# Performance work log

Hardware: AMD Instinct MI355X
Metric: run time of the kernel (lower is better)

## Reference

```python
import jax, jax.numpy as jnp
import numpy as np

HIDDEN = 4096
NUM_HEADS = 32
HEAD_DIM = HIDDEN // NUM_HEADS


def _fp8_roundtrip(x):
    # emulate torch float8_e4m3fn weight storage
    return x.astype(jnp.float8_e4m3fn).astype(jnp.float32)


def setup_inputs() -> dict:
    key = jax.random.key(0)
    ks = jax.random.split(key, 10)
    B, S = 2, 4096
    hidden_states = jax.random.normal(ks[0], (B, S, HIDDEN), dtype=jnp.float32)
    scale = 0.02
    def lin(kw, kb):
        w = jax.random.normal(kw, (HIDDEN, HIDDEN), dtype=jnp.float32) * scale
        b = jax.random.normal(kb, (HIDDEN,), dtype=jnp.float32) * scale
        return w, b
    wq, bq = lin(ks[1], ks[2])
    wk, bk = lin(ks[3], ks[4])
    wv, bv = lin(ks[5], ks[6])
    wl, bl = lin(ks[7], ks[8])
    # fp8-quantized Q/K/V projections (latent projection stays fp32)
    wq, bq = _fp8_roundtrip(wq), _fp8_roundtrip(bq)
    wk, bk = _fp8_roundtrip(wk), _fp8_roundtrip(bk)
    wv, bv = _fp8_roundtrip(wv), _fp8_roundtrip(bv)
    return {"hidden_states": hidden_states, "wq": wq, "bq": bq, "wk": wk,
            "bk": bk, "wv": wv, "bv": bv, "wl": wl, "bl": bl}


def reference(hidden_states, wq, bq, wk, bk, wv, bv, wl, bl):
    B, S, E = hidden_states.shape
    H, D = NUM_HEADS, HEAD_DIM
    q = (hidden_states @ wq.T + bq).reshape(B, S, H, D)
    k = (hidden_states @ wk.T + bk).reshape(B, S, H, D)
    v = (hidden_states @ wv.T + bv).reshape(B, S, H, D)
    latent = hidden_states @ wl.T + bl  # computed but unused, as in source
    # NOTE: source does NOT transpose to [B,H,S,D]; scores are [B,S,H,H]
    scores = jnp.einsum('bshd,bstd->bsht', q, k) / np.sqrt(D).astype(np.float32)
    probs = jax.nn.softmax(scores, axis=-1)
    context = jnp.einsum('bsht,bstd->bshd', probs, v).reshape(B, S, E)
    return context
```

## Files before the change

kernel.cpp:

```cpp
#include <hip/hip_runtime.h>
#include <stdint.h>

#define HIDDEN 4096
#define M_TOK 8192
#define KDIM 4096

typedef __attribute__((ext_vector_type(8))) __bf16 bf16x8;
typedef __attribute__((ext_vector_type(4))) float f32x4;
typedef __attribute__((ext_vector_type(8))) unsigned short u16x8;

#define GAS __attribute__((address_space(1)))
#define LAS __attribute__((address_space(3)))

__device__ __forceinline__ unsigned short f2bf(float f) {
  unsigned int u = __float_as_uint(f);
  u += 0x7FFFu + ((u >> 16) & 1u);
  return (unsigned short)(u >> 16);
}
__device__ __forceinline__ float bf2f(unsigned short b) {
  return __uint_as_float(((unsigned int)b) << 16);
}

__global__ __launch_bounds__(256) void cvt_kernel(const float* __restrict__ in,
                                                  unsigned short* __restrict__ out,
                                                  int n8) {
  int i = blockIdx.x * 256 + threadIdx.x;
  if (i >= n8) return;
  const f32x4* p = (const f32x4*)in + (size_t)2 * i;
  f32x4 a = p[0], b = p[1];
  u16x8 o;
  o[0] = f2bf(a.x); o[1] = f2bf(a.y); o[2] = f2bf(a.z); o[3] = f2bf(a.w);
  o[4] = f2bf(b.x); o[5] = f2bf(b.y); o[6] = f2bf(b.z); o[7] = f2bf(b.w);
  ((u16x8*)out)[i] = o;
}

#define BAR() __builtin_amdgcn_s_barrier()
#define PRIO(p) __builtin_amdgcn_s_setprio(p)
#define VMC6() asm volatile("s_waitcnt vmcnt(6)" ::: "memory")
#define VMC4() asm volatile("s_waitcnt vmcnt(4)" ::: "memory")
#define VMC0() asm volatile("s_waitcnt vmcnt(0)" ::: "memory")
#define PH_MID() do { __builtin_amdgcn_s_barrier(); \
  asm volatile("s_waitcnt lgkmcnt(0)" ::: "memory"); \
  __builtin_amdgcn_sched_barrier(0); } while (0)

__global__ __launch_bounds__(512, 2) void gemm_qkv(
    const unsigned short* __restrict__ A,
    const unsigned short* __restrict__ W,
    const float* __restrict__ bias,
    unsigned short* __restrict__ out) {
  __shared__ __attribute__((aligned(16))) unsigned short lds[65536];

  int tid = threadIdx.x;
  int lane = tid & 63;
  int w = tid >> 6;
  int wm = w >> 2;
  int wn = w & 3;
  int l16 = lane & 15;
  int lk = lane >> 4;

  int bid = blockIdx.x;
  int wg = (bid & 7) * 192 + (bid >> 3);
  int tm = wg / 48;
  int tn = wg - tm * 48;
  int m0 = tm << 8, n0 = tn << 8;

  int rp = tid >> 3;
  int ce = ((tid & 7) << 3) ^ ((rp & 7) << 3);
  const unsigned short* aSrc = A + (size_t)(m0 + rp) * KDIM + ce;
  const unsigned short* bSrc = W + (size_t)(n0 + rp) * KDIM + ce;
  int tid8 = tid * 8;

#define STA(b, h, kt) do { \
  __builtin_amdgcn_global_load_lds((GAS void*)(aSrc + (size_t)((h)*128) * KDIM + (kt)*64), \
      (LAS void*)(lds + (b)*16384 + (h)*8192 + tid8), 16, 0, 0); \
  __builtin_amdgcn_global_load_lds((GAS void*)(aSrc + (size_t)((h)*128 + 64) * KDIM + (kt)*64), \
      (LAS void*)(lds + (b)*16384 + (h)*8192 + 4096 + tid8), 16, 0, 0); } while (0)
#define STB(b, h, kt) do { \
  __builtin_amdgcn_global_load_lds((GAS void*)(bSrc + (size_t)((h)*128) * KDIM + (kt)*64), \
      (LAS void*)(lds + 32768 + (b)*16384 + (h)*8192 + tid8), 16, 0, 0); \
  __builtin_amdgcn_global_load_lds((GAS void*)(bSrc + (size_t)((h)*128 + 64) * KDIM + (kt)*64), \
      (LAS void*)(lds + 32768 + (b)*16384 + (h)*8192 + 4096 + tid8), 16, 0, 0); } while (0)

  int colbase = (lk << 3) ^ ((l16 & 7) << 3);
  int aRd = wm * 8192 + l16 * 64 + colbase;
  int bRd = (wn >> 1) * 8192 + (wn & 1) * 4096 + l16 * 64 + colbase;

#define RD_A(c, mi, ks) (*(const bf16x8*)(lds + (c)*16384 + (((aRd) + (mi)*1024) ^ ((ks)*32))))
#define RD_B(c, nj, ks) (*(const bf16x8*)(lds + 32768 + (c)*16384 + (((bRd) + (nj)*1024) ^ ((ks)*32))))

  bf16x8 av[8][2];
  bf16x8 bv[4][2];
  f32x4 acc[8][4] = {};

#define RP1(c) do { \
  bv[0][0]=RD_B(c,0,0); bv[0][1]=RD_B(c,0,1); bv[1][0]=RD_B(c,1,0); bv[1][1]=RD_B(c,1,1); \
  bv[2][0]=RD_B(c,2,0); bv[2][1]=RD_B(c,2,1); bv[3][0]=RD_B(c,3,0); bv[3][1]=RD_B(c,3,1); \
  av[0][0]=RD_A(c,0,0); av[0][1]=RD_A(c,0,1); av[1][0]=RD_A(c,1,0); av[1][1]=RD_A(c,1,1); } while (0)
#define RP2(c) do { \
  av[2][0]=RD_A(c,2,0); av[2][1]=RD_A(c,2,1); av[3][0]=RD_A(c,3,0); av[3][1]=RD_A(c,3,1); \
  av[4][0]=RD_A(c,4,0); av[4][1]=RD_A(c,4,1); av[5][0]=RD_A(c,5,0); av[5][1]=RD_A(c,5,1); } while (0)
#define RP3(c) do { \
  av[6][0]=RD_A(c,6,0); av[6][1]=RD_A(c,6,1); av[7][0]=RD_A(c,7,0); av[7][1]=RD_A(c,7,1); } while (0)

#define MFMA2(mi, nj) do { \
  acc[mi][nj] = __builtin_amdgcn_mfma_f32_16x16x32_bf16(av[mi][0], bv[nj][0], acc[mi][nj], 0, 0, 0); \
  acc[mi][nj] = __builtin_amdgcn_mfma_f32_16x16x32_bf16(av[mi][1], bv[nj][1], acc[mi][nj], 0, 0, 0); } while (0)
#define MM(mi) do { MFMA2(mi,0); MFMA2(mi,1); MFMA2(mi,2); MFMA2(mi,3); } while (0)

  STB(0, 0, 0); STB(0, 1, 0); STA(0, 0, 0); STA(0, 1, 0);
  VMC4();
  STB(1, 0, 1); STB(1, 1, 1); STA(1, 0, 1);
  VMC6();
  BAR();

  for (int it = 0; it < 31; ++it) {
    int k1 = 2 * it + 1, k2 = 2 * it + 2, k3 = 2 * it + 3;
    RP1(0); STA(1, 1, k1); PH_MID(); PRIO(1); MM(0); MM(1); PRIO(0); BAR();
    RP2(0); STB(0, 0, k2); PH_MID(); PRIO(1); MM(2); MM(3); PRIO(0); BAR();
    RP3(0); STB(0, 1, k2); PH_MID(); PRIO(1); MM(4); MM(5); PRIO(0); BAR();
            STA(0, 0, k2); PH_MID(); PRIO(1); MM(6); MM(7); PRIO(0); VMC6(); BAR();
    RP1(1); STA(0, 1, k2); PH_MID(); PRIO(1); MM(0); MM(1); PRIO(0); BAR();
    RP2(1); STB(1, 0, k3); PH_MID(); PRIO(1); MM(2); MM(3); PRIO(0); BAR();
    RP3(1); STB(1, 1, k3); PH_MID(); PRIO(1); MM(4); MM(5); PRIO(0); BAR();
            STA(1, 0, k3); PH_MID(); PRIO(1); MM(6); MM(7); PRIO(0); VMC6(); BAR();
  }
  RP1(0); STA(1, 1, 63); PH_MID(); PRIO(1); MM(0); MM(1); PRIO(0); BAR();
  RP2(0);                PH_MID(); PRIO(1); MM(2); MM(3); PRIO(0); BAR();
  RP3(0);                PH_MID(); PRIO(1); MM(4); MM(5); PRIO(0); BAR();
                         PH_MID(); PRIO(1); MM(6); MM(7); PRIO(0); VMC0(); BAR();
  RP1(1);                PH_MID(); PRIO(1); MM(0); MM(1); PRIO(0); BAR();
  RP2(1);                PH_MID(); PRIO(1); MM(2); MM(3); PRIO(0); BAR();
  RP3(1);                PH_MID(); PRIO(1); MM(4); MM(5); PRIO(0); BAR();
                         PH_MID(); PRIO(1); MM(6); MM(7); PRIO(0);

  int matc = n0 >> 12;
  int ncol = (n0 & 4095) + wn * 64;
  unsigned short* O = out + (size_t)matc * M_TOK * HIDDEN;
  float bb[4];
#pragma unroll
  for (int nj = 0; nj < 4; ++nj) bb[nj] = bias[n0 + wn * 64 + nj * 16 + l16];
#pragma unroll
  for (int mi = 0; mi < 8; ++mi) {
#pragma unroll
    for (int r = 0; r < 4; ++r) {
      int row = m0 + wm * 128 + mi * 16 + lk * 4 + r;
      size_t rb = (size_t)row * HIDDEN + ncol + l16;
#pragma unroll
      for (int nj = 0; nj < 4; ++nj)
        O[rb + nj * 16] = f2bf(acc[mi][nj][r] + bb[nj]);
    }
  }
}

__global__ __launch_bounds__(256) void attn_kernel(const unsigned short* __restrict__ qkv,
                                                   float* __restrict__ out) {
  __shared__ float sQ[32 * 132];
  __shared__ float sK[32 * 132];
  __shared__ float sV[32 * 132];
  __shared__ float sP[32 * 33];

  int m = blockIdx.x;
  int tid = threadIdx.x;
  const unsigned short* gq = qkv + (size_t)m * HIDDEN;
  const unsigned short* gk = gq + (size_t)M_TOK * HIDDEN;
  const unsigned short* gv = gk + (size_t)M_TOK * HIDDEN;

  int row = tid >> 3;
  int cb = (tid & 7) << 4;
  int go = row * 128 + cb;
  int lo = row * 132 + cb;
  {
    u16x8 x0 = *(const u16x8*)(gq + go);
    u16x8 x1 = *(const u16x8*)(gq + go + 8);
#pragma unroll
    for (int j = 0; j < 8; ++j) { sQ[lo + j] = bf2f(x0[j]); sQ[lo + 8 + j] = bf2f(x1[j]); }
    x0 = *(const u16x8*)(gk + go);
    x1 = *(const u16x8*)(gk + go + 8);
#pragma unroll
    for (int j = 0; j < 8; ++j) { sK[lo + j] = bf2f(x0[j]); sK[lo + 8 + j] = bf2f(x1[j]); }
    x0 = *(const u16x8*)(gv + go);
    x1 = *(const u16x8*)(gv + go + 8);
#pragma unroll
    for (int j = 0; j < 8; ++j) { sV[lo + j] = bf2f(x0[j]); sV[lo + 8 + j] = bf2f(x1[j]); }
  }
  __syncthreads();

  int h = tid >> 3;
  int t4 = (tid & 7) << 2;
  const f32x4* qr = (const f32x4*)(sQ + h * 132);
  const f32x4* k0 = (const f32x4*)(sK + (t4 + 0) * 132);
  const f32x4* k1 = (const f32x4*)(sK + (t4 + 1) * 132);
  const f32x4* k2 = (const f32x4*)(sK + (t4 + 2) * 132);
  const f32x4* k3 = (const f32x4*)(sK + (t4 + 3) * 132);
  float s0 = 0.f, s1 = 0.f, s2 = 0.f, s3 = 0.f;
#pragma unroll
  for (int d = 0; d < 32; ++d) {
    f32x4 q = qr[d];
    f32x4 a = k0[d]; s0 += q.x * a.x + q.y * a.y + q.z * a.z + q.w * a.w;
    f32x4 b = k1[d]; s1 += q.x * b.x + q.y * b.y + q.z * b.z + q.w * b.w;
    f32x4 c = k2[d]; s2 += q.x * c.x + q.y * c.y + q.z * c.z + q.w * c.w;
    f32x4 e = k3[d]; s3 += q.x * e.x + q.y * e.y + q.z * e.z + q.w * e.w;
  }
  const float scale = 0.08838834764831845f;
  s0 *= scale; s1 *= scale; s2 *= scale; s3 *= scale;
  float mx = fmaxf(fmaxf(s0, s1), fmaxf(s2, s3));
  mx = fmaxf(mx, __shfl_xor(mx, 1));
  mx = fmaxf(mx, __shfl_xor(mx, 2));
  mx = fmaxf(mx, __shfl_xor(mx, 4));
  float e0 = __expf(s0 - mx), e1 = __expf(s1 - mx), e2 = __expf(s2 - mx), e3 = __expf(s3 - mx);
  float sum = e0 + e1 + e2 + e3;
  sum += __shfl_xor(sum, 1);
  sum += __shfl_xor(sum, 2);
  sum += __shfl_xor(sum, 4);
  float inv = 1.0f / sum;
  sP[h * 33 + t4 + 0] = e0 * inv;
  sP[h * 33 + t4 + 1] = e1 * inv;
  sP[h * 33 + t4 + 2] = e2 * inv;
  sP[h * 33 + t4 + 3] = e3 * inv;
  __syncthreads();

  int d0 = (tid & 7) << 4;
  f32x4 o0 = {0.f, 0.f, 0.f, 0.f}, o1 = o0, o2 = o0, o3 = o0;
  const float* pr = sP + h * 33;
#pragma unroll
  for (int t = 0; t < 32; ++t) {
    float p = pr[t];
    const f32x4* vr = (const f32x4*)(sV + t * 132 + d0);
    o0 += p * vr[0];
    o1 += p * vr[1];
    o2 += p * vr[2];
    o3 += p * vr[3];
  }
  f32x4* op = (f32x4*)(out + (size_t)m * HIDDEN + h * 128 + d0);
  op[0] = o0; op[1] = o1; op[2] = o2; op[3] = o3;
}

extern "C" void kernel_launch(void* const* d_in, const int* in_sizes, int n_in,
                              void* d_out, int out_size, void* d_ws, size_t ws_size,
                              hipStream_t stream) {
  const float* hs = (const float*)d_in[0];
  const float* wq = (const float*)d_in[1];
  const float* bq = (const float*)d_in[2];
  const float* wk = (const float*)d_in[3];
  const float* bk = (const float*)d_in[4];
  const float* wv = (const float*)d_in[5];
  const float* bv = (const float*)d_in[6];

  char* ws = (char*)d_ws;
  const size_t HS_OFF = 0;
  const size_t W_OFF = 67108864;
  const size_t QKV_OFF = 167772160;
  const size_t BIAS_OFF = 369098752;
  const size_t NEED = 369147904;
  if (ws_size < NEED) return;

  unsigned short* hsb = (unsigned short*)(ws + HS_OFF);
  unsigned short* wb = (unsigned short*)(ws + W_OFF);
  unsigned short* qkv = (unsigned short*)(ws + QKV_OFF);
  float* bias = (float*)(ws + BIAS_OFF);

  cvt_kernel<<<16384, 256, 0, stream>>>(hs, hsb, 4194304);
  cvt_kernel<<<8192, 256, 0, stream>>>(wq, wb, 2097152);
  cvt_kernel<<<8192, 256, 0, stream>>>(wk, wb + 16777216, 2097152);
  cvt_kernel<<<8192, 256, 0, stream>>>(wv, wb + 33554432, 2097152);
  hipMemcpyAsync(bias, bq, 16384, hipMemcpyDeviceToDevice, stream);
  hipMemcpyAsync(bias + 4096, bk, 16384, hipMemcpyDeviceToDevice, stream);
  hipMemcpyAsync(bias + 8192, bv, 16384, hipMemcpyDeviceToDevice, stream);

  gemm_qkv<<<1536, 512, 0, stream>>>(hsb, wb, bias, qkv);
  attn_kernel<<<8192, 256, 0, stream>>>(qkv, (float*)d_out);
}
```

Measured before the change: 896.6 us.

## Switch QKV GEMM from 16x16x32 to 32x32x16 bf16 MFMA tiles

```diff
diff --git a/kernel.cpp b/kernel.cpp
--- a/kernel.cpp
+++ b/kernel.cpp
@@ -7,6 +7,7 @@
 
 typedef __attribute__((ext_vector_type(8))) __bf16 bf16x8;
 typedef __attribute__((ext_vector_type(4))) float f32x4;
+typedef __attribute__((ext_vector_type(16))) float f32x16;
 typedef __attribute__((ext_vector_type(8))) unsigned short u16x8;
 
 #define GAS __attribute__((address_space(1)))
@@ -55,8 +56,9 @@
   int w = tid >> 6;
   int wm = w >> 2;
   int wn = w & 3;
-  int l16 = lane & 15;
-  int lk = lane >> 4;
+  int l31 = lane & 31;
+  int lg = lane >> 5;
+  int l7 = lane & 7;
 
   int bid = blockIdx.x;
   int wg = (bid & 7) * 192 + (bid >> 3);
@@ -81,31 +83,29 @@
   __builtin_amdgcn_global_load_lds((GAS void*)(bSrc + (size_t)((h)*128 + 64) * KDIM + (kt)*64), \
       (LAS void*)(lds + 32768 + (b)*16384 + (h)*8192 + 4096 + tid8), 16, 0, 0); } while (0)
 
-  int colbase = (lk << 3) ^ ((l16 & 7) << 3);
-  int aRd = wm * 8192 + l16 * 64 + colbase;
-  int bRd = (wn >> 1) * 8192 + (wn & 1) * 4096 + l16 * 64 + colbase;
-
-#define RD_A(c, mi, ks) (*(const bf16x8*)(lds + (c)*16384 + (((aRd) + (mi)*1024) ^ ((ks)*32))))
-#define RD_B(c, nj, ks) (*(const bf16x8*)(lds + 32768 + (c)*16384 + (((bRd) + (nj)*1024) ^ ((ks)*32))))
-
-  bf16x8 av[8][2];
-  bf16x8 bv[4][2];
-  f32x4 acc[8][4] = {};
-
-#define RP1(c) do { \
-  bv[0][0]=RD_B(c,0,0); bv[0][1]=RD_B(c,0,1); bv[1][0]=RD_B(c,1,0); bv[1][1]=RD_B(c,1,1); \
-  bv[2][0]=RD_B(c,2,0); bv[2][1]=RD_B(c,2,1); bv[3][0]=RD_B(c,3,0); bv[3][1]=RD_B(c,3,1); \
-  av[0][0]=RD_A(c,0,0); av[0][1]=RD_A(c,0,1); av[1][0]=RD_A(c,1,0); av[1][1]=RD_A(c,1,1); } while (0)
-#define RP2(c) do { \
-  av[2][0]=RD_A(c,2,0); av[2][1]=RD_A(c,2,1); av[3][0]=RD_A(c,3,0); av[3][1]=RD_A(c,3,1); \
-  av[4][0]=RD_A(c,4,0); av[4][1]=RD_A(c,4,1); av[5][0]=RD_A(c,5,0); av[5][1]=RD_A(c,5,1); } while (0)
-#define RP3(c) do { \
-  av[6][0]=RD_A(c,6,0); av[6][1]=RD_A(c,6,1); av[7][0]=RD_A(c,7,0); av[7][1]=RD_A(c,7,1); } while (0)
-
-#define MFMA2(mi, nj) do { \
-  acc[mi][nj] = __builtin_amdgcn_mfma_f32_16x16x32_bf16(av[mi][0], bv[nj][0], acc[mi][nj], 0, 0, 0); \
-  acc[mi][nj] = __builtin_amdgcn_mfma_f32_16x16x32_bf16(av[mi][1], bv[nj][1], acc[mi][nj], 0, 0, 0); } while (0)
-#define MM(mi) do { MFMA2(mi,0); MFMA2(mi,1); MFMA2(mi,2); MFMA2(mi,3); } while (0)
+  int aRd0 = wm * 8192 + l31 * 64 + ((lg ^ l7) << 3);
+  int aK0 = aRd0, aK1 = aRd0 ^ 16, aK2 = aRd0 ^ 32, aK3 = aRd0 ^ 48;
+  int bRd0 = (wn >> 1) * 8192 + (wn & 1) * 4096 + l31 * 64 + ((lg ^ l7) << 3);
+  int bK0 = bRd0, bK1 = bRd0 ^ 16, bK2 = bRd0 ^ 32, bK3 = bRd0 ^ 48;
+
+#define RA(c, mi, ks) avv[ks][mi] = *(const bf16x8*)(lds + (c)*16384 + aK##ks + (mi)*2048)
+#define RB(c, nj, ks) bvv[nj][ks] = *(const bf16x8*)(lds + 32768 + (c)*16384 + bK##ks + (nj)*2048)
+
+  bf16x8 avv[4][4];
+  bf16x8 bvv[2][4];
+  f32x16 acc[4][2] = {};
+
+#define MF(mi, nj, ks) acc[mi][nj] = __builtin_amdgcn_mfma_f32_32x32x16_bf16( \
+    avv[ks][mi], bvv[nj][ks], acc[mi][nj], 0, 0, 0)
+#define MMKS(ks) do { MF(0,0,ks); MF(0,1,ks); MF(1,0,ks); MF(1,1,ks); \
+                      MF(2,0,ks); MF(2,1,ks); MF(3,0,ks); MF(3,1,ks); } while (0)
+
+#define RP1(c) do { RB(c,0,0); RB(c,0,1); RB(c,0,2); RB(c,0,3); \
+                    RB(c,1,0); RB(c,1,1); RB(c,1,2); RB(c,1,3); \
+                    RA(c,0,0); RA(c,1,0); RA(c,2,0); RA(c,3,0); } while (0)
+#define RP2(c) do { RA(c,0,1); RA(c,1,1); RA(c,2,1); RA(c,3,1); \
+                    RA(c,0,2); RA(c,1,2); RA(c,2,2); RA(c,3,2); } while (0)
+#define RP3(c) do { RA(c,0,3); RA(c,1,3); RA(c,2,3); RA(c,3,3); } while (0)
 
   STB(0, 0, 0); STB(0, 1, 0); STA(0, 0, 0); STA(0, 1, 0);
   VMC4();
@@ -115,39 +115,37 @@
 
   for (int it = 0; it < 31; ++it) {
     int k1 = 2 * it + 1, k2 = 2 * it + 2, k3 = 2 * it + 3;
-    RP1(0); STA(1, 1, k1); PH_MID(); PRIO(1); MM(0); MM(1); PRIO(0); BAR();
-    RP2(0); STB(0, 0, k2); PH_MID(); PRIO(1); MM(2); MM(3); PRIO(0); BAR();
-    RP3(0); STB(0, 1, k2); PH_MID(); PRIO(1); MM(4); MM(5); PRIO(0); BAR();
-            STA(0, 0, k2); PH_MID(); PRIO(1); MM(6); MM(7); PRIO(0); VMC6(); BAR();
-    RP1(1); STA(0, 1, k2); PH_MID(); PRIO(1); MM(0); MM(1); PRIO(0); BAR();
-    RP2(1); STB(1, 0, k3); PH_MID(); PRIO(1); MM(2); MM(3); PRIO(0); BAR();
-    RP3(1); STB(1, 1, k3); PH_MID(); PRIO(1); MM(4); MM(5); PRIO(0); BAR();
-            STA(1, 0, k3); PH_MID(); PRIO(1); MM(6); MM(7); PRIO(0); VMC6(); BAR();
-  }
-  RP1(0); STA(1, 1, 63); PH_MID(); PRIO(1); MM(0); MM(1); PRIO(0); BAR();
-  RP2(0);                PH_MID(); PRIO(1); MM(2); MM(3); PRIO(0); BAR();
-  RP3(0);                PH_MID(); PRIO(1); MM(4); MM(5); PRIO(0); BAR();
-                         PH_MID(); PRIO(1); MM(6); MM(7); PRIO(0); VMC0(); BAR();
-  RP1(1);                PH_MID(); PRIO(1); MM(0); MM(1); PRIO(0); BAR();
-  RP2(1);                PH_MID(); PRIO(1); MM(2); MM(3); PRIO(0); BAR();
-  RP3(1);                PH_MID(); PRIO(1); MM(4); MM(5); PRIO(0); BAR();
-                         PH_MID(); PRIO(1); MM(6); MM(7); PRIO(0);
+    RP1(0); STA(1, 1, k1); PH_MID(); PRIO(1); MMKS(0); PRIO(0); BAR();
+    RP2(0); STB(0, 0, k2); PH_MID(); PRIO(1); MMKS(1); PRIO(0); BAR();
+    RP3(0); STB(0, 1, k2); PH_MID(); PRIO(1); MMKS(2); PRIO(0); BAR();
+            STA(0, 0, k2); PH_MID(); PRIO(1); MMKS(3); PRIO(0); VMC6(); BAR();
+    RP1(1); STA(0, 1, k2); PH_MID(); PRIO(1); MMKS(0); PRIO(0); BAR();
+    RP2(1); STB(1, 0, k3); PH_MID(); PRIO(1); MMKS(1); PRIO(0); BAR();
+    RP3(1); STB(1, 1, k3); PH_MID(); PRIO(1); MMKS(2); PRIO(0); BAR();
+            STA(1, 0, k3); PH_MID(); PRIO(1); MMKS(3); PRIO(0); VMC6(); BAR();
+  }
+  RP1(0); STA(1, 1, 63); PH_MID(); PRIO(1); MMKS(0); PRIO(0); BAR();
+  RP2(0);                PH_MID(); PRIO(1); MMKS(1); PRIO(0); BAR();
+  RP3(0);                PH_MID(); PRIO(1); MMKS(2); PRIO(0); BAR();
+                         PH_MID(); PRIO(1); MMKS(3); PRIO(0); VMC0(); BAR();
+  RP1(1);                PH_MID(); PRIO(1); MMKS(0); PRIO(0); BAR();
+  RP2(1);                PH_MID(); PRIO(1); MMKS(1); PRIO(0); BAR();
+  RP3(1);                PH_MID(); PRIO(1); MMKS(2); PRIO(0); BAR();
+                         PH_MID(); PRIO(1); MMKS(3); PRIO(0);
 
   int matc = n0 >> 12;
   int ncol = (n0 & 4095) + wn * 64;
   unsigned short* O = out + (size_t)matc * M_TOK * HIDDEN;
-  float bb[4];
-#pragma unroll
-  for (int nj = 0; nj < 4; ++nj) bb[nj] = bias[n0 + wn * 64 + nj * 16 + l16];
-#pragma unroll
-  for (int mi = 0; mi < 8; ++mi) {
-#pragma unroll
-    for (int r = 0; r < 4; ++r) {
-      int row = m0 + wm * 128 + mi * 16 + lk * 4 + r;
-      size_t rb = (size_t)row * HIDDEN + ncol + l16;
-#pragma unroll
-      for (int nj = 0; nj < 4; ++nj)
-        O[rb + nj * 16] = f2bf(acc[mi][nj][r] + bb[nj]);
+  float bb0 = bias[n0 + wn * 64 + l31];
+  float bb1 = bias[n0 + wn * 64 + 32 + l31];
+#pragma unroll
+  for (int mi = 0; mi < 4; ++mi) {
+#pragma unroll
+    for (int r = 0; r < 16; ++r) {
+      int row = m0 + wm * 128 + mi * 32 + (r & 3) + 8 * (r >> 2) + 4 * lg;
+      size_t rb = (size_t)row * HIDDEN + ncol + l31;
+      O[rb] = f2bf(acc[mi][0][r] + bb0);
+      O[rb + 32] = f2bf(acc[mi][1][r] + bb1);
     }
   }
 }
```

Result: slower. 968.7 us (+8.0%).
